# Kernel optimization log

Measured on AMD Instinct MI355X. Metric: run time of the kernel, lower is better.

## Reference

```python
import jax, jax.numpy as jnp
import numpy as np

ALPHA = 0.2
NEG_INF = -9e15


def setup_inputs() -> dict:
    key = jax.random.key(0)
    k1, k2, k3, k4 = jax.random.split(key, 4)
    N, F_IN, F_OUT, H = 4096, 1, 64, 12
    x = jax.random.normal(k1, (N, F_IN), dtype=jnp.float32)
    adj = jax.random.randint(k2, (N, N), 0, 2).astype(jnp.int32)
    # per-head params stacked: W [H, F_IN, F_OUT], a [H, 2*F_OUT, 1]
    W = jax.random.normal(k3, (H, F_IN, F_OUT), dtype=jnp.float32) * 0.1
    a = jax.random.normal(k4, (H, 2 * F_OUT, 1), dtype=jnp.float32) * 0.1
    return {"x": x, "adj": adj, "W": W, "a": a}


def reference(x, adj, W, a):
    # h per head: [H, N, F_OUT]
    h = jnp.einsum('nf,hfo->hno', x, W)
    F_out = h.shape[-1]
    # a_input[i,j] = concat(h_i, h_j), so a_input @ a = h_i.a_src + h_j.a_dst
    a_src = a[:, :F_out, 0]   # [H, F_OUT]
    a_dst = a[:, F_out:, 0]   # [H, F_OUT]
    e_src = jnp.einsum('hnf,hf->hn', h, a_src)  # [H, N]
    e_dst = jnp.einsum('hnf,hf->hn', h, a_dst)  # [H, N]
    e = jax.nn.leaky_relu(e_src[:, :, None] + e_dst[:, None, :], ALPHA)  # [H,N,N]
    e = jnp.where(adj[None] > 0, e, NEG_INF)
    attn = jax.nn.softmax(e, axis=-1)           # softmax over neighbors j
    h_prime = jnp.einsum('hij,hjf->hif', attn, h)  # [H, N, F_OUT]
    # concat heads along feature dim -> [N, H*F_OUT]
    N = h_prime.shape[1]
    return jnp.transpose(h_prime, (1, 0, 2)).reshape(N, -1)
```

## Files before the change

### kernel.cpp

```cpp
#include <hip/hip_runtime.h>

#define GAT_H 12
#define GAT_N 4096
#define GAT_F 64
#define GAT_HALF 2048
#define LOG2E 1.4426950408889634f

__global__ __launch_bounds__(64) void gat_prep(const float* __restrict__ W,
                                               const float* __restrict__ a,
                                               const float* __restrict__ x,
                                               float* __restrict__ sd) {
    const int b = blockIdx.x;
    const int f = threadIdx.x;
    if (b < GAT_H) {
        const float wf = W[b * GAT_F + f];
        float ps = wf * a[b * 2 * GAT_F + f];
        float pd = wf * a[b * 2 * GAT_F + GAT_F + f];
        #pragma unroll
        for (int off = 32; off > 0; off >>= 1) {
            ps += __shfl_xor(ps, off, 64);
            pd += __shfl_xor(pd, off, 64);
        }
        if (f == 0) { sd[b] = ps; sd[GAT_H + b] = pd; }
    } else {
        float s = 0.0f;
        #pragma unroll
        for (int j = 0; j < GAT_N / 64; ++j) s += x[j * 64 + f];
        #pragma unroll
        for (int off = 32; off > 0; off >>= 1) s += __shfl_xor(s, off, 64);
        if (f == 0) sd[2 * GAT_H] = s * (1.0f / GAT_N);
    }
}

__global__ __launch_bounds__(256) void gat_main(const float* __restrict__ x,
                                                const int* __restrict__ adj,
                                                const float* __restrict__ W,
                                                const float* __restrict__ sd,
                                                float* __restrict__ out) {
    __shared__ float xs[GAT_N];
    __shared__ float part[2][2][GAT_H][2];
    __shared__ float cbuf[2][GAT_H];

    const int tid = threadIdx.x;
    #pragma unroll
    for (int it = 0; it < GAT_N / (256 * 4); ++it) {
        ((float4*)xs)[it * 256 + tid] = ((const float4*)x)[it * 256 + tid];
    }
    __syncthreads();

    const int lane = tid & 63;
    const int wave = tid >> 6;
    const int rloc = wave >> 1;
    const int half = wave & 1;
    const int row  = blockIdx.x * 2 + rloc;
    const float xi = xs[row];

    float b1[GAT_H], d1[GAT_H];
    #pragma unroll
    for (int h = 0; h < GAT_H; ++h) {
        b1[h] = xi * sd[h] * LOG2E;
        d1[h] = sd[GAT_H + h] * LOG2E;
    }
    float den[GAT_H], num[GAT_H];
    #pragma unroll
    for (int h = 0; h < GAT_H; ++h) { den[h] = 0.0f; num[h] = 0.0f; }

    const int4*   __restrict__ adjrow =
        (const int4*)(adj + (size_t)row * GAT_N + half * GAT_HALF);
    const float4* __restrict__ xs4 = (const float4*)(xs + half * GAT_HALF);

    int4   a4 = adjrow[lane];
    float4 x4 = xs4[lane];
    #pragma unroll 1
    for (int it = 0; it < 8; ++it) {
        const int nxt = (it < 7 ? it + 1 : 7) * 64 + lane;
        int4   a4n = adjrow[nxt];
        float4 x4n = xs4[nxt];
        #pragma unroll
        for (int e = 0; e < 4; ++e) {
            const int   ai = (e == 0) ? a4.x : (e == 1) ? a4.y : (e == 2) ? a4.z : a4.w;
            const float xj = (e == 0) ? x4.x : (e == 1) ? x4.y : (e == 2) ? x4.z : x4.w;
            const float mb = (ai > 0) ? 0.0f : -12800.0f;
            #pragma unroll
            for (int h = 0; h < GAT_H; ++h) {
                const float q   = fmaf(xj, d1[h], b1[h]);
                const float t   = fmaf(0.6f, q, mb);
                const float arg = fmaf(0.4f, fabsf(q), t);
                const float p   = __builtin_amdgcn_exp2f(arg);
                den[h] += p;
                num[h] = fmaf(p, xj, num[h]);
            }
        }
        a4 = a4n; x4 = x4n;
    }

    #pragma unroll
    for (int h = 0; h < GAT_H; ++h) {
        #pragma unroll
        for (int off = 32; off > 0; off >>= 1) {
            den[h] += __shfl_xor(den[h], off, 64);
            num[h] += __shfl_xor(num[h], off, 64);
        }
    }
    if (lane == 0) {
        #pragma unroll
        for (int h = 0; h < GAT_H; ++h) {
            part[rloc][half][h][0] = den[h];
            part[rloc][half][h][1] = num[h];
        }
    }
    __syncthreads();

    if (tid < 2 * GAT_H) {
        const int r = (tid >= GAT_H) ? 1 : 0;
        const int h = tid - r * GAT_H;
        const float dsum = part[r][0][h][0] + part[r][1][h][0];
        const float nsum = part[r][0][h][1] + part[r][1][h][1];
        cbuf[r][h] = dsum > 0.0f ? nsum / dsum : sd[2 * GAT_H];
    }
    __syncthreads();

    #pragma unroll
    for (int r = 0; r < 2; ++r) {
        const size_t base = (size_t)(blockIdx.x * 2 + r) * (GAT_H * GAT_F);
        #pragma unroll
        for (int k = 0; k < 3; ++k) {
            const int pos = k * 256 + tid;
            out[base + pos] = cbuf[r][pos >> 6] * W[pos];
        }
    }
}

extern "C" void kernel_launch(void* const* d_in, const int* in_sizes, int n_in,
                              void* d_out, int out_size, void* d_ws, size_t ws_size,
                              hipStream_t stream) {
    const float* x   = (const float*)d_in[0];
    const int*   adj = (const int*)d_in[1];
    const float* W   = (const float*)d_in[2];
    const float* a   = (const float*)d_in[3];
    float* out = (float*)d_out;
    float* sd  = (float*)d_ws;

    gat_prep<<<13, 64, 0, stream>>>(W, a, x, sd);
    gat_main<<<GAT_N / 2, 256, 0, stream>>>(x, adj, W, sd, out);
}
```

Measured before the change: 128.3 us.

## Factor exp of leaky-relu into precomputed per-node tables and process four rows per block

Because F_IN is 1, the attention logit is separable, so exp(leaky_relu(s_i + d_j)) becomes max(E1[j], rho_i * E2[j]). The prep kernel now builds per-head float2 exp tables over all nodes. The main kernel swaps the per-edge exp2 for a multiply and max, and masks with FMA against a 0/1 neighbor mask. Each block now handles four rows so the table loads are reused across rows, with waves split by head group and column half. In exchange, the kernel reads an extra table from global memory each iteration and drops the max-subtraction safety of the earlier exp formulation.

Result: slower. 143.9 us (+12.2%).

```diff
diff --git a/kernel.cpp b/kernel.cpp
--- a/kernel.cpp
+++ b/kernel.cpp
@@ -3,126 +3,187 @@
 #define GAT_H 12
 #define GAT_N 4096
 #define GAT_F 64
-#define GAT_HALF 2048
 #define LOG2E 1.4426950408889634f
 
-__global__ __launch_bounds__(64) void gat_prep(const float* __restrict__ W,
-                                               const float* __restrict__ a,
-                                               const float* __restrict__ x,
-                                               float* __restrict__ sd) {
-    const int b = blockIdx.x;
-    const int f = threadIdx.x;
-    if (b < GAT_H) {
-        const float wf = W[b * GAT_F + f];
-        float ps = wf * a[b * 2 * GAT_F + f];
-        float pd = wf * a[b * 2 * GAT_F + GAT_F + f];
-        #pragma unroll
-        for (int off = 32; off > 0; off >>= 1) {
-            ps += __shfl_xor(ps, off, 64);
-            pd += __shfl_xor(pd, off, 64);
-        }
-        if (f == 0) { sd[b] = ps; sd[GAT_H + b] = pd; }
-    } else {
-        float s = 0.0f;
-        #pragma unroll
-        for (int j = 0; j < GAT_N / 64; ++j) s += x[j * 64 + f];
-        #pragma unroll
-        for (int off = 32; off > 0; off >>= 1) s += __shfl_xor(s, off, 64);
-        if (f == 0) sd[2 * GAT_H] = s * (1.0f / GAT_N);
-    }
-}
-
-__global__ __launch_bounds__(256) void gat_main(const float* __restrict__ x,
-                                                const int* __restrict__ adj,
-                                                const float* __restrict__ W,
-                                                const float* __restrict__ sd,
-                                                float* __restrict__ out) {
-    __shared__ float xs[GAT_N];
-    __shared__ float part[2][2][GAT_H][2];
-    __shared__ float cbuf[2][GAT_H];
-
-    const int tid = threadIdx.x;
-    #pragma unroll
-    for (int it = 0; it < GAT_N / (256 * 4); ++it) {
-        ((float4*)xs)[it * 256 + tid] = ((const float4*)x)[it * 256 + tid];
-    }
-    __syncthreads();
-
+
+__device__ float2 g_tab[GAT_H * GAT_N];
+__device__ float  g_sd[2 * GAT_H + 1];
+
+__global__ __launch_bounds__(256) void gat_prep(const float* __restrict__ W,
+                                                const float* __restrict__ a,
+                                                const float* __restrict__ x) {
+    const int b    = blockIdx.x;
+    const int tid  = threadIdx.x;
     const int lane = tid & 63;
     const int wave = tid >> 6;
-    const int rloc = wave >> 1;
-    const int half = wave & 1;
-    const int row  = blockIdx.x * 2 + rloc;
-    const float xi = xs[row];
-
-    float b1[GAT_H], d1[GAT_H];
-    #pragma unroll
-    for (int h = 0; h < GAT_H; ++h) {
-        b1[h] = xi * sd[h] * LOG2E;
-        d1[h] = sd[GAT_H + h] * LOG2E;
-    }
-    float den[GAT_H], num[GAT_H];
-    #pragma unroll
-    for (int h = 0; h < GAT_H; ++h) { den[h] = 0.0f; num[h] = 0.0f; }
-
-    const int4*   __restrict__ adjrow =
-        (const int4*)(adj + (size_t)row * GAT_N + half * GAT_HALF);
-    const float4* __restrict__ xs4 = (const float4*)(xs + half * GAT_HALF);
-
-    int4   a4 = adjrow[lane];
-    float4 x4 = xs4[lane];
-    #pragma unroll 1
-    for (int it = 0; it < 8; ++it) {
-        const int nxt = (it < 7 ? it + 1 : 7) * 64 + lane;
-        int4   a4n = adjrow[nxt];
-        float4 x4n = xs4[nxt];
-        #pragma unroll
-        for (int e = 0; e < 4; ++e) {
-            const int   ai = (e == 0) ? a4.x : (e == 1) ? a4.y : (e == 2) ? a4.z : a4.w;
-            const float xj = (e == 0) ? x4.x : (e == 1) ? x4.y : (e == 2) ? x4.z : x4.w;
-            const float mb = (ai > 0) ? 0.0f : -12800.0f;
-            #pragma unroll
-            for (int h = 0; h < GAT_H; ++h) {
-                const float q   = fmaf(xj, d1[h], b1[h]);
-                const float t   = fmaf(0.6f, q, mb);
-                const float arg = fmaf(0.4f, fabsf(q), t);
-                const float p   = __builtin_amdgcn_exp2f(arg);
-                den[h] += p;
-                num[h] = fmaf(p, xj, num[h]);
-            }
-        }
-        a4 = a4n; x4 = x4n;
-    }
-
-    #pragma unroll
-    for (int h = 0; h < GAT_H; ++h) {
-        #pragma unroll
-        for (int off = 32; off > 0; off >>= 1) {
-            den[h] += __shfl_xor(den[h], off, 64);
-            num[h] += __shfl_xor(num[h], off, 64);
-        }
-    }
-    if (lane == 0) {
-        #pragma unroll
-        for (int h = 0; h < GAT_H; ++h) {
-            part[rloc][half][h][0] = den[h];
-            part[rloc][half][h][1] = num[h];
-        }
+
+    if (b < GAT_H) {
+        if (wave == 0) {
+            const float wf = W[b * GAT_F + lane];
+            float ps = wf * a[b * 2 * GAT_F + lane];
+            float pd = wf * a[b * 2 * GAT_F + GAT_F + lane];
+            #pragma unroll
+            for (int off = 32; off > 0; off >>= 1) {
+                ps += __shfl_xor(ps, off, 64);
+                pd += __shfl_xor(pd, off, 64);
+            }
+            if (lane == 0) { g_sd[b] = ps; g_sd[GAT_H + b] = pd; }
+        }
+        return;
+    }
+    if (b == GAT_H) {
+        if (wave == 0) {
+            float s = 0.0f;
+            #pragma unroll
+            for (int j = 0; j < GAT_N / 64; ++j) s += x[j * 64 + lane];
+            #pragma unroll
+            for (int off = 32; off > 0; off >>= 1) s += __shfl_xor(s, off, 64);
+            if (lane == 0) g_sd[2 * GAT_H] = s * (1.0f / GAT_N);
+        }
+        return;
+    }
+
+    const int bt    = b - (GAT_H + 1);
+    const int h     = bt >> 2;
+    const int chunk = bt & 3;
+    const float wf  = W[h * GAT_F + lane];
+    float pd = wf * a[h * 2 * GAT_F + GAT_F + lane];
+    #pragma unroll
+    for (int off = 32; off > 0; off >>= 1) pd += __shfl_xor(pd, off, 64);
+    const float dl = pd * LOG2E;
+    #pragma unroll
+    for (int k = 0; k < 4; ++k) {
+        const int j   = chunk * 1024 + k * 256 + tid;
+        const float t = dl * x[j];
+        g_tab[h * GAT_N + j] = make_float2(__builtin_amdgcn_exp2f(t),
+                                           __builtin_amdgcn_exp2f(0.2f * t));
+    }
+}
+
+__global__ __launch_bounds__(256, 4) void gat_main(const float* __restrict__ x,
+                                                   const int* __restrict__ adj,
+                                                   const float* __restrict__ W,
+                                                   float* __restrict__ out) {
+    __shared__ float xs[GAT_N];
+    __shared__ float rho_s[4][16];
+    __shared__ float part[2][2][4][6][2];
+    __shared__ float cbuf[4][GAT_H];
+
+    const int tid  = threadIdx.x;
+    const int row0 = blockIdx.x * 4;
+
+    #pragma unroll
+    for (int it = 0; it < GAT_N / (256 * 4); ++it)
+        ((float4*)xs)[it * 256 + tid] = ((const float4*)x)[it * 256 + tid];
+    if (tid < 64) {
+        const int r = tid >> 4, hh = tid & 15;
+        if (hh < GAT_H)
+            rho_s[r][hh] =
+                __builtin_amdgcn_exp2f(-0.8f * LOG2E * x[row0 + r] * g_sd[hh]);
     }
     __syncthreads();
 
-    if (tid < 2 * GAT_H) {
-        const int r = (tid >= GAT_H) ? 1 : 0;
-        const int h = tid - r * GAT_H;
-        const float dsum = part[r][0][h][0] + part[r][1][h][0];
-        const float nsum = part[r][0][h][1] + part[r][1][h][1];
-        cbuf[r][h] = dsum > 0.0f ? nsum / dsum : sd[2 * GAT_H];
+    const int lane  = tid & 63;
+    const int wave  = tid >> 6;
+    const int hg    = wave >> 1;
+    const int jh    = wave & 1;
+    const int hbase = hg * 6;
+    const int jb    = jh * 2048 + lane;
+
+    float rho[4][6];
+    #pragma unroll
+    for (int r = 0; r < 4; ++r)
+        #pragma unroll
+        for (int hh = 0; hh < 6; ++hh)
+            rho[r][hh] = __uint_as_float(__builtin_amdgcn_readfirstlane(
+                __float_as_uint(rho_s[r][hbase + hh])));
+
+    float den[4][6], num[4][6];
+    #pragma unroll
+    for (int r = 0; r < 4; ++r)
+        #pragma unroll
+        for (int hh = 0; hh < 6; ++hh) { den[r][hh] = 0.0f; num[r][hh] = 0.0f; }
+
+    const int*    __restrict__ adp = adj + (size_t)row0 * GAT_N + jb;
+    const float2* __restrict__ tb  = g_tab + hbase * GAT_N + jb;
+
+    int    a_c[4];
+    float2 E_c[6];
+    float  x_c;
+    #pragma unroll
+    for (int r = 0; r < 4; ++r)  a_c[r]  = adp[r * GAT_N];
+    #pragma unroll
+    for (int hh = 0; hh < 6; ++hh) E_c[hh] = tb[hh * GAT_N];
+    x_c = xs[jb];
+
+    #pragma unroll 2
+    for (int e = 0; e < 32; ++e) {
+        const int eo = (e < 31 ? e + 1 : 31) * 64;
+        int    a_n[4];
+        float2 E_n[6];
+        #pragma unroll
+        for (int r = 0; r < 4; ++r)   a_n[r]  = adp[r * GAT_N + eo];
+        #pragma unroll
+        for (int hh = 0; hh < 6; ++hh) E_n[hh] = tb[hh * GAT_N + eo];
+        const float x_n = xs[jb + eo];
+
+        float m[4], mxj[4];
+        #pragma unroll
+        for (int r = 0; r < 4; ++r) {
+            const bool nb = a_c[r] > 0;
+            m[r]   = nb ? 1.0f : 0.0f;
+            mxj[r] = nb ? x_c  : 0.0f;
+        }
+        #pragma unroll
+        for (int hh = 0; hh < 6; ++hh) {
+            const float e1 = E_c[hh].x, e2 = E_c[hh].y;
+            #pragma unroll
+            for (int r = 0; r < 4; ++r) {
+                const float p = fmaxf(e1, rho[r][hh] * e2);
+                den[r][hh] = fmaf(p, m[r],   den[r][hh]);
+                num[r][hh] = fmaf(p, mxj[r], num[r][hh]);
+            }
+        }
+        #pragma unroll
+        for (int r = 0; r < 4; ++r)   a_c[r]  = a_n[r];
+        #pragma unroll
+        for (int hh = 0; hh < 6; ++hh) E_c[hh] = E_n[hh];
+        x_c = x_n;
+    }
+
+    #pragma unroll
+    for (int r = 0; r < 4; ++r) {
+        #pragma unroll
+        for (int hh = 0; hh < 6; ++hh) {
+            float d = den[r][hh], n = num[r][hh];
+            #pragma unroll
+            for (int off = 32; off > 0; off >>= 1) {
+                d += __shfl_xor(d, off, 64);
+                n += __shfl_xor(n, off, 64);
+            }
+            if (lane == 0) {
+                part[jh][hg][r][hh][0] = d;
+                part[jh][hg][r][hh][1] = n;
+            }
+        }
     }
     __syncthreads();
 
-    #pragma unroll
-    for (int r = 0; r < 2; ++r) {
-        const size_t base = (size_t)(blockIdx.x * 2 + r) * (GAT_H * GAT_F);
+    if (tid < 64) {
+        const int r = tid >> 4, h = tid & 15;
+        if (h < GAT_H) {
+            const int g  = (h >= 6) ? 1 : 0;
+            const int hh = h - 6 * g;
+            const float dsum = part[0][g][r][hh][0] + part[1][g][r][hh][0];
+            const float nsum = part[0][g][r][hh][1] + part[1][g][r][hh][1];
+            cbuf[r][h] = dsum > 0.0f ? nsum / dsum : g_sd[2 * GAT_H];
+        }
+    }
+    __syncthreads();
+
+    #pragma unroll
+    for (int r = 0; r < 4; ++r) {
+        const size_t base = (size_t)(row0 + r) * (GAT_H * GAT_F);
         #pragma unroll
         for (int k = 0; k < 3; ++k) {
             const int pos = k * 256 + tid;
@@ -139,8 +200,8 @@
     const float* W   = (const float*)d_in[2];
     const float* a   = (const float*)d_in[3];
     float* out = (float*)d_out;
-    float* sd  = (float*)d_ws;
-
-    gat_prep<<<13, 64, 0, stream>>>(W, a, x, sd);
-    gat_main<<<GAT_N / 2, 256, 0, stream>>>(x, adj, W, sd, out);
+    (void)d_ws; (void)ws_size;
+
+    gat_prep<<<GAT_H + 1 + 48, 256, 0, stream>>>(W, a, x);
+    gat_main<<<GAT_N / 4, 256, 0, stream>>>(x, adj, W, out);
 }
```
